# Performance work log

Measured on AMD Instinct MI355X. Metric: run time of the kernel, lower is better.

Reference implementation:

```python
import jax, jax.numpy as jnp
import numpy as np

L, MODS, D, R, B, T = 2, 3, 512, 32, 16, 512  # nlayers, n_modals, embed_dim, rank, batch, length
BETA = 0.1


def setup_inputs() -> dict:
    key = jax.random.key(0)
    ks = jax.random.split(key, 12)
    s_in = 1.0 / np.sqrt(D)      # nn.Linear default init scale for d->R projections
    s_att = 1.0 / np.sqrt(R * R)  # for (R*R)->d projection

    def w(k, shape, scale):
        return jax.random.uniform(k, shape, jnp.float32, -scale, scale)

    return {
        "x_a": jax.random.normal(ks[0], (B, T, D), jnp.float32),
        "x_t": jax.random.normal(ks[1], (B, T, D), jnp.float32),
        "x_v": jax.random.normal(ks[2], (B, T, D), jnp.float32),
        # stacked per-layer, per-modality params
        "Wq1": w(ks[3], (L, MODS, D, R), s_in), "bq1": w(ks[4], (L, MODS, R), s_in),
        "Wq2": w(ks[5], (L, MODS, D, R), s_in), "bq2": w(ks[6], (L, MODS, R), s_in),
        "Wk1": w(ks[7], (L, MODS, D, R), s_in), "bk1": w(ks[8], (L, MODS, R), s_in),
        "Wk2": w(ks[9], (L, MODS, D, R), s_in), "bk2": w(ks[10], (L, MODS, R), s_in),
        "Watt": w(ks[11], (L, MODS, R * R, D), s_att),
        "batt": jnp.zeros((L, MODS, D), jnp.float32),
    }


def _proj(X, W, b):
    # X: [M,B,T,D], W: [M,D,R], b: [M,R] -> [M,B,T,R]
    return jnp.einsum('mbtd,mdr->mbtr', X, W) + b[:, None, None, :]


def reference(x_a, x_t, x_v, Wq1, bq1, Wq2, bq2, Wk1, bk1, Wk2, bk2, Watt, batt):
    X = jnp.stack([x_a, x_t, x_v])  # [M,B,T,D]
    for li in range(L):
        q1 = _proj(X, Wq1[li], bq1[li])
        q2 = _proj(X, Wq2[li], bq2[li])
        k1 = _proj(X, Wk1[li], bk1[li])
        k2 = _proj(X, Wk2[li], bk2[li])
        # low-rank bilinear maps: G_qk[j] = (q1 outer q2) * (k1 outer k2) -> [M,B,T,R,R]
        G = (q1[..., :, None] * q2[..., None, :]) * (k1[..., :, None] * k2[..., None, :])
        Mqk = G.mean(axis=2)  # [M,B,R,R] mean over time
        outs = []
        for j in range(MODS):
            # chained cross-modal contraction == G_j @ (prod_{l!=j, ascending} M_l)
            P = None
            for l in range(MODS):
                if l == j:
                    continue
                P = Mqk[l] if P is None else jnp.einsum('bkl,blo->bko', P, Mqk[l])
            att = jnp.einsum('btkl,blo->btko', G[j], P)  # [B,T,R,R]
            flat = att.reshape(B, T, R * R)
            proj = flat @ Watt[li, j] + batt[li, j]  # [B,T,D]
            outs.append(proj * X[j] + BETA * X[j])  # residual combine (dropout is eval-mode identity)
        X = jnp.stack(outs)
    return X[0], X[1], X[2]
```

## Files before the change

### kernel.cpp

```cpp
#include <hip/hip_runtime.h>

#define L_ 2
#define MODS_ 3
#define D_ 512
#define R_ 32
#define B_ 16
#define T_ 512
#define BT_ (B_*T_)
#define BETA_ 0.1f

typedef _Float16 h8 __attribute__((ext_vector_type(8)));
typedef __fp16   fp16x2 __attribute__((ext_vector_type(2)));
typedef float f32x16 __attribute__((ext_vector_type(16)));

typedef __attribute__((address_space(3))) unsigned int lds_u32;
typedef __attribute__((address_space(1))) const unsigned int glb_u32;

__device__ __forceinline__ void gload_lds16(const uint4* gsrc, uint4* ldst){
    __builtin_amdgcn_global_load_lds((glb_u32*)gsrc, (lds_u32*)ldst, 16, 0, 0);
}

__device__ __forceinline__ h8 mk_h8(float f0,float f1,float f2,float f3,
                                    float f4,float f5,float f6,float f7){
    union { h8 v; fp16x2 p[4]; } r;
    r.p[0] = __builtin_amdgcn_cvt_pkrtz(f0,f1);
    r.p[1] = __builtin_amdgcn_cvt_pkrtz(f2,f3);
    r.p[2] = __builtin_amdgcn_cvt_pkrtz(f4,f5);
    r.p[3] = __builtin_amdgcn_cvt_pkrtz(f6,f7);
    return r.v;
}

__global__ __launch_bounds__(256) void k_cvt(
    const float* __restrict__ Watt,
    const float* __restrict__ Wq1, const float* __restrict__ Wk1,
    const float* __restrict__ Wq2, const float* __restrict__ Wk2,
    uint4* __restrict__ WattF, uint4* __restrict__ WprojF)
{
    const int t = blockIdx.x*256 + threadIdx.x;
    const int NWATT = 6*32*16*2*64;
    if (t < NWATT) {
        const int lane = t & 63, f = t >> 6;
        const int kh = f & 1, nb = (f>>1)&15, s = (f>>5)&31, lj = f>>10;
        const int col  = nb*32 + (lane&31);
        const int row0 = s*32 + kh*16 + (lane>>5)*8;
        const float* src = Watt + ((size_t)lj*1024)*D_ + col;
        union { uint4 q; unsigned short us[8]; } o;
        #pragma unroll
        for (int i=0;i<8;i++){
            float x = src[(size_t)(row0+i)*D_];
            o.us[i] = __builtin_bit_cast(unsigned short, (_Float16)x);
        }
        WattF[t] = o.q;
    } else {
        const int t2 = t - NWATT;
        const int lane = t2 & 63, f = t2 >> 6;
        const int nb = f & 3, s = (f>>2)&31, lm = f>>7;
        const float* Ws = (nb==0)?Wq1:(nb==1)?Wk1:(nb==2)?Wq2:Wk2;
        const int r  = lane&31;
        const int k0 = s*16 + (lane>>5)*8;
        const float* src = Ws + ((size_t)lm*D_)*R_ + r;
        union { uint4 q; unsigned short us[8]; } o;
        #pragma unroll
        for (int i=0;i<8;i++){
            float x = src[(size_t)(k0+i)*R_];
            o.us[i] = __builtin_bit_cast(unsigned short, (_Float16)x);
        }
        WprojF[t2] = o.q;
    }
}

__global__ __launch_bounds__(256) void k_proj_mfma(
    const float* __restrict__ X, const uint4* __restrict__ WprojF,
    const float* __restrict__ bq1, const float* __restrict__ bq2,
    const float* __restrict__ bk1, const float* __restrict__ bk2,
    float* __restrict__ U, float* __restrict__ V, int li)
{
    __shared__ uint4 sm[2][256];
    const int tid = threadIdx.x;
    const int wid = tid>>6, lane = tid&63;
    const int lh = lane>>5, lr = lane&31;
    const int tokg = wid&1, colh = wid>>1;
    const int m = blockIdx.y;
    const int tok0 = blockIdx.x*64;
    const int lm = li*MODS_ + m;
    const int t = tok0 + tokg*32 + lr;

    const uint4* src  = WprojF + (size_t)lm*8192;
    const float* Xrow = X + ((size_t)m*BT_ + t)*D_;

    f32x16 acc0, acc1;
    #pragma unroll
    for (int i=0;i<16;i++){ acc0[i]=0.f; acc1[i]=0.f; }

    gload_lds16(src + tid, &sm[0][wid*64]);
    __syncthreads();

    float4 x0 = *(const float4*)&Xrow[lh*8];
    float4 x1 = *(const float4*)&Xrow[lh*8+4];

    #pragma unroll
    for (int s=0;s<32;s++){
        const int cur = s&1;
        float4 nx0, nx1;
        if (s<31){
            gload_lds16(src + (s+1)*256 + tid, &sm[cur^1][wid*64]);
            nx0 = *(const float4*)&Xrow[(s+1)*16 + lh*8];
            nx1 = *(const float4*)&Xrow[(s+1)*16 + lh*8 + 4];
        }
        h8 a  = mk_h8(x0.x,x0.y,x0.z,x0.w, x1.x,x1.y,x1.z,x1.w);
        h8 b0 = __builtin_bit_cast(h8, sm[cur][(colh*2+0)*64 + lane]);
        h8 b1 = __builtin_bit_cast(h8, sm[cur][(colh*2+1)*64 + lane]);
        acc0 = __builtin_amdgcn_mfma_f32_32x32x16_f16(a, b0, acc0, 0,0,0);
        acc1 = __builtin_amdgcn_mfma_f32_32x32x16_f16(a, b1, acc1, 0,0,0);
        __syncthreads();
        if (s<31){ x0 = nx0; x1 = nx1; }
    }

    const float bA = (colh==0 ? bq1 : bq2)[lm*R_ + lr];
    const float bB = (colh==0 ? bk1 : bk2)[lm*R_ + lr];
    float* Out = (colh==0 ? U : V);
    #pragma unroll
    for (int reg=0;reg<16;reg++){
        const int row = (reg&3) + 8*(reg>>2) + 4*lh;
        const int tt  = tok0 + tokg*32 + row;
        Out[((size_t)m*BT_ + tt)*R_ + lr] = (acc0[reg]+bA)*(acc1[reg]+bB);
    }
}

__global__ __launch_bounds__(256) void k_mqk(const float* __restrict__ U,
                                             const float* __restrict__ V,
                                             float* __restrict__ Mqk)
{
    const int tid = threadIdx.x;
    const int mb  = blockIdx.x;

    __shared__ float Us[64][32];
    __shared__ float Vs[64][32];

    const int l = tid & 31;
    const int g = tid >> 5;
    float acc[4] = {0.f, 0.f, 0.f, 0.f};

    const float* Ub = U + (size_t)mb * T_ * R_;
    const float* Vb = V + (size_t)mb * T_ * R_;
    const int st = tid >> 2, sc = (tid & 3) * 8;

    for (int t0 = 0; t0 < T_; t0 += 64) {
        const float4 u0 = *(const float4*)&Ub[(size_t)(t0 + st) * R_ + sc];
        const float4 u1 = *(const float4*)&Ub[(size_t)(t0 + st) * R_ + sc + 4];
        const float4 v0 = *(const float4*)&Vb[(size_t)(t0 + st) * R_ + sc];
        const float4 v1 = *(const float4*)&Vb[(size_t)(t0 + st) * R_ + sc + 4];
        __syncthreads();
        *(float4*)&Us[st][sc]     = u0; *(float4*)&Us[st][sc + 4] = u1;
        *(float4*)&Vs[st][sc]     = v0; *(float4*)&Vs[st][sc + 4] = v1;
        __syncthreads();
        #pragma unroll
        for (int tt = 0; tt < 64; ++tt) {
            const float v = Vs[tt][l];
            #pragma unroll
            for (int i = 0; i < 4; ++i) acc[i] += Us[tt][g + 8 * i] * v;
        }
    }
    #pragma unroll
    for (int i = 0; i < 4; ++i)
        Mqk[(size_t)mb * (R_ * R_) + (size_t)(g + 8 * i) * R_ + l] = acc[i] * (1.0f / T_);
}

__global__ __launch_bounds__(256) void k_pmat(const float* __restrict__ Mqk,
                                              float* __restrict__ P)
{
    const int tid = threadIdx.x;
    const int j = blockIdx.x, b = blockIdx.y;
    const int a = (j == 0) ? 1 : 0;
    const int c = (j == 2) ? 1 : 2;

    __shared__ float As[32][32];
    __shared__ float Cs[32][32];

    const float4 av = *(const float4*)&Mqk[((size_t)(a * B_ + b)) * 1024 + tid * 4];
    const float4 cv = *(const float4*)&Mqk[((size_t)(c * B_ + b)) * 1024 + tid * 4];
    *(float4*)&(((float*)As)[tid * 4]) = av;
    *(float4*)&(((float*)Cs)[tid * 4]) = cv;
    __syncthreads();

    const int o = tid & 31, g = tid >> 5;
    float acc[4] = {0.f, 0.f, 0.f, 0.f};
    #pragma unroll
    for (int l = 0; l < 32; ++l) {
        const float cvv = Cs[l][o];
        #pragma unroll
        for (int i = 0; i < 4; ++i) acc[i] += As[g + 8 * i][l] * cvv;
    }
    #pragma unroll
    for (int i = 0; i < 4; ++i)
        P[((size_t)(j * B_ + b)) * 1024 + (size_t)(g + 8 * i) * R_ + o] = acc[i];
}

__global__ __launch_bounds__(256) void k_wvec(const float* __restrict__ V,
                                              const float* __restrict__ P,
                                              float* __restrict__ W2)
{
    const int tid  = threadIdx.x;
    const int m    = blockIdx.y;
    const int tok0 = blockIdx.x * 128;
    const int b    = tok0 / T_;

    __shared__ float Ps[32][32];
    __shared__ float Vs[128][32];

    *(float4*)&(((float*)Ps)[tid * 4]) =
        *(const float4*)&P[((size_t)(m * B_ + b)) * 1024 + tid * 4];

    const int st = tid >> 1, sc = (tid & 1) * 16;
    const float* Vb = V + ((size_t)m * BT_ + tok0) * R_;
    #pragma unroll
    for (int q = 0; q < 4; ++q)
        *(float4*)&Vs[st][sc + q * 4] = *(const float4*)&Vb[(size_t)st * R_ + sc + q * 4];
    __syncthreads();

    const int o = tid & 31, g = tid >> 5;
    float* W2b = W2 + ((size_t)m * BT_ + tok0) * R_;
    #pragma unroll
    for (int i = 0; i < 16; ++i) {
        const int t = g * 16 + i;
        float acc = 0.f;
        #pragma unroll
        for (int l = 0; l < 32; ++l) acc += Vs[t][l] * Ps[l][o];
        W2b[(size_t)t * R_ + o] = acc;
    }
}

__global__ __launch_bounds__(256) void k_gemm2_mfma(
    const float* __restrict__ U, const float* __restrict__ W2,
    const uint4* __restrict__ WattF, const float* __restrict__ batt,
    float* __restrict__ X, int li)
{
    __shared__ uint4 sm[2][1024];
    const int tid = threadIdx.x;
    const int wid = tid>>6, lane = tid&63;
    const int lh = lane>>5, lr = lane&31;
    const int tokg = wid&1, colg = wid>>1;
    const int j = blockIdx.z;
    const int tok0 = blockIdx.x*64;
    const int nbB = blockIdx.y*8;
    const int t = tok0 + tokg*32 + lr;

    const uint4* src = WattF + (size_t)(li*MODS_ + j)*65536 + (size_t)nbB*128;

    const float* Urow = U  + ((size_t)j*BT_ + t)*R_;
    const float* Wrow = W2 + ((size_t)j*BT_ + t)*R_;
    float u_r[32];
    #pragma unroll
    for (int q=0;q<8;q++){
        float4 t4 = *(const float4*)&Urow[q*4];
        u_r[q*4+0]=t4.x; u_r[q*4+1]=t4.y; u_r[q*4+2]=t4.z; u_r[q*4+3]=t4.w;
    }
    const float4 wa0 = *(const float4*)&Wrow[lh*8];
    const float4 wa1 = *(const float4*)&Wrow[lh*8+4];
    const float4 wb0 = *(const float4*)&Wrow[16+lh*8];
    const float4 wb1 = *(const float4*)&Wrow[16+lh*8+4];

    f32x16 acc[4];
    #pragma unroll
    for (int n=0;n<4;n++){
        #pragma unroll
        for (int i=0;i<16;i++) acc[n][i]=0.f;
    }

    #pragma unroll
    for (int it=0;it<4;it++)
        gload_lds16(src + it*256 + tid, &sm[0][it*256 + wid*64]);
    __syncthreads();

    #pragma unroll
    for (int s=0;s<32;s++){
        const int cur = s&1;
        if (s<31){
            const uint4* ssrc = src + (size_t)(s+1)*2048;
            #pragma unroll
            for (int it=0;it<4;it++)
                gload_lds16(ssrc + it*256 + tid, &sm[cur^1][it*256 + wid*64]);
        }
        const float us = u_r[s];
        h8 a0 = mk_h8(us*wa0.x,us*wa0.y,us*wa0.z,us*wa0.w,
                      us*wa1.x,us*wa1.y,us*wa1.z,us*wa1.w);
        h8 a1 = mk_h8(us*wb0.x,us*wb0.y,us*wb0.z,us*wb0.w,
                      us*wb1.x,us*wb1.y,us*wb1.z,us*wb1.w);
        #pragma unroll
        for (int n=0;n<4;n++){
            h8 b0 = __builtin_bit_cast(h8, sm[cur][(colg*4+n)*128 +      lane]);
            h8 b1 = __builtin_bit_cast(h8, sm[cur][(colg*4+n)*128 + 64 + lane]);
            acc[n] = __builtin_amdgcn_mfma_f32_32x32x16_f16(a0, b0, acc[n], 0,0,0);
            acc[n] = __builtin_amdgcn_mfma_f32_32x32x16_f16(a1, b1, acc[n], 0,0,0);
        }
        __syncthreads();
    }

    const float* battp = batt + (size_t)(li*MODS_ + j)*D_;
    #pragma unroll
    for (int n=0;n<4;n++){
        const int d  = (nbB + colg*4 + n)*32 + lr;
        const float bt = battp[d];
        #pragma unroll
        for (int reg=0; reg<16; ++reg){
            const int row = (reg&3) + 8*(reg>>2) + 4*lh;
            const size_t xi = ((size_t)j*BT_ + tok0 + tokg*32 + row)*D_ + d;
            const float xv = X[xi];
            X[xi] = (acc[n][reg] + bt)*xv + BETA_*xv;
        }
    }
}

extern "C" void kernel_launch(void* const* d_in, const int* in_sizes, int n_in,
                              void* d_out, int out_size, void* d_ws, size_t ws_size,
                              hipStream_t stream)
{
    const float* x_a  = (const float*)d_in[0];
    const float* x_t  = (const float*)d_in[1];
    const float* x_v  = (const float*)d_in[2];
    const float* Wq1  = (const float*)d_in[3];
    const float* bq1  = (const float*)d_in[4];
    const float* Wq2  = (const float*)d_in[5];
    const float* bq2  = (const float*)d_in[6];
    const float* Wk1  = (const float*)d_in[7];
    const float* bk1  = (const float*)d_in[8];
    const float* Wk2  = (const float*)d_in[9];
    const float* bk2  = (const float*)d_in[10];
    const float* Watt = (const float*)d_in[11];
    const float* batt = (const float*)d_in[12];

    float* X  = (float*)d_out;
    float* U  = (float*)d_ws;
    float* V  = U  + (size_t)MODS_ * BT_ * R_;
    float* W2 = V  + (size_t)MODS_ * BT_ * R_;
    float* Mq = W2 + (size_t)MODS_ * BT_ * R_;
    float* P  = Mq + (size_t)MODS_ * B_ * R_ * R_;
    uint4* WattF  = (uint4*)(P + (size_t)MODS_ * B_ * R_ * R_);
    uint4* WprojF = WattF + 393216;

    const size_t modbytes = (size_t)BT_ * D_ * sizeof(float);
    (void)hipMemcpyAsync(X,                        x_a, modbytes, hipMemcpyDeviceToDevice, stream);
    (void)hipMemcpyAsync(X + (size_t)BT_ * D_,     x_t, modbytes, hipMemcpyDeviceToDevice, stream);
    (void)hipMemcpyAsync(X + (size_t)2 * BT_ * D_, x_v, modbytes, hipMemcpyDeviceToDevice, stream);

    k_cvt<<<1728, 256, 0, stream>>>(Watt, Wq1, Wk1, Wq2, Wk2, WattF, WprojF);

    for (int li = 0; li < L_; ++li) {
        k_proj_mfma<<<dim3(BT_/64, MODS_), 256, 0, stream>>>(
            X, WprojF, bq1, bq2, bk1, bk2, U, V, li);
        k_mqk<<<dim3(MODS_ * B_), 256, 0, stream>>>(U, V, Mq);
        k_pmat<<<dim3(MODS_, B_), 256, 0, stream>>>(Mq, P);
        k_wvec<<<dim3(BT_/128, MODS_), 256, 0, stream>>>(V, P, W2);
        k_gemm2_mfma<<<dim3(BT_/64, D_/256, MODS_), 256, 0, stream>>>(
            U, W2, WattF, batt, X, li);
    }
}
```

Baseline: 318.3 us.

## Store intermediates in fp16, split mqk over time, drop input copies and LDS staging

Stores the U, V and W2 intermediates as scaled fp16 instead of fp32, which cuts their memory traffic. The time-mean reduction is split across eight partial blocks, with the summing folded into k_pmat. Layer 0 reads the input tensors directly, so the three device memcpys go away. Both MFMA kernels now load weights straight into registers with double buffering instead of staging them through LDS behind barriers. The fixed 64x scale factors add an fp16 overflow or precision risk, and register pressure rises in the gemm2 kernel.

```diff
diff --git a/kernel.cpp b/kernel.cpp
--- a/kernel.cpp
+++ b/kernel.cpp
@@ -13,13 +13,6 @@
 typedef __fp16   fp16x2 __attribute__((ext_vector_type(2)));
 typedef float f32x16 __attribute__((ext_vector_type(16)));
 
-typedef __attribute__((address_space(3))) unsigned int lds_u32;
-typedef __attribute__((address_space(1))) const unsigned int glb_u32;
-
-__device__ __forceinline__ void gload_lds16(const uint4* gsrc, uint4* ldst){
-    __builtin_amdgcn_global_load_lds((glb_u32*)gsrc, (lds_u32*)ldst, 16, 0, 0);
-}
-
 __device__ __forceinline__ h8 mk_h8(float f0,float f1,float f2,float f3,
                                     float f4,float f5,float f6,float f7){
     union { h8 v; fp16x2 p[4]; } r;
@@ -28,6 +21,13 @@
     r.p[2] = __builtin_amdgcn_cvt_pkrtz(f4,f5);
     r.p[3] = __builtin_amdgcn_cvt_pkrtz(f6,f7);
     return r.v;
+}
+
+__device__ __forceinline__ float h2f(unsigned short x){
+    return (float)__builtin_bit_cast(_Float16, x);
+}
+__device__ __forceinline__ unsigned short f2h(float x){
+    return __builtin_bit_cast(unsigned short, (_Float16)x);
 }
 
 __global__ __launch_bounds__(256) void k_cvt(
@@ -46,10 +46,7 @@
         const float* src = Watt + ((size_t)lj*1024)*D_ + col;
         union { uint4 q; unsigned short us[8]; } o;
         #pragma unroll
-        for (int i=0;i<8;i++){
-            float x = src[(size_t)(row0+i)*D_];
-            o.us[i] = __builtin_bit_cast(unsigned short, (_Float16)x);
-        }
+        for (int i=0;i<8;i++) o.us[i] = f2h(src[(size_t)(row0+i)*D_]);
         WattF[t] = o.q;
     } else {
         const int t2 = t - NWATT;
@@ -61,21 +58,19 @@
         const float* src = Ws + ((size_t)lm*D_)*R_ + r;
         union { uint4 q; unsigned short us[8]; } o;
         #pragma unroll
-        for (int i=0;i<8;i++){
-            float x = src[(size_t)(k0+i)*R_];
-            o.us[i] = __builtin_bit_cast(unsigned short, (_Float16)x);
-        }
+        for (int i=0;i<8;i++) o.us[i] = f2h(src[(size_t)(k0+i)*R_]);
         WprojF[t2] = o.q;
     }
 }
 
 __global__ __launch_bounds__(256) void k_proj_mfma(
-    const float* __restrict__ X, const uint4* __restrict__ WprojF,
+    const float* __restrict__ xa, const float* __restrict__ xt,
+    const float* __restrict__ xv, const float* __restrict__ X,
+    const uint4* __restrict__ WprojF,
     const float* __restrict__ bq1, const float* __restrict__ bq2,
     const float* __restrict__ bk1, const float* __restrict__ bk2,
-    float* __restrict__ U, float* __restrict__ V, int li)
-{
-    __shared__ uint4 sm[2][256];
+    unsigned short* __restrict__ U16, unsigned short* __restrict__ V16, int li)
+{
     const int tid = threadIdx.x;
     const int wid = tid>>6, lane = tid&63;
     const int lh = lane>>5, lr = lane&31;
@@ -85,120 +80,122 @@
     const int lm = li*MODS_ + m;
     const int t = tok0 + tokg*32 + lr;
 
-    const uint4* src  = WprojF + (size_t)lm*8192;
-    const float* Xrow = X + ((size_t)m*BT_ + t)*D_;
+    const float* Xbase = (li==0) ? (m==0?xa:(m==1?xt:xv)) : (X + (size_t)m*BT_*D_);
+    const float* Xrow  = Xbase + (size_t)t*D_;
+    const uint4* src   = WprojF + (size_t)lm*8192 + (colh*2)*64 + lane;
 
     f32x16 acc0, acc1;
     #pragma unroll
     for (int i=0;i<16;i++){ acc0[i]=0.f; acc1[i]=0.f; }
 
-    gload_lds16(src + tid, &sm[0][wid*64]);
-    __syncthreads();
-
+    uint4 bc0 = src[0], bc1 = src[64];
+    uint4 bn0, bn1;
     float4 x0 = *(const float4*)&Xrow[lh*8];
     float4 x1 = *(const float4*)&Xrow[lh*8+4];
+    float4 nx0, nx1;
 
     #pragma unroll
     for (int s=0;s<32;s++){
-        const int cur = s&1;
-        float4 nx0, nx1;
         if (s<31){
-            gload_lds16(src + (s+1)*256 + tid, &sm[cur^1][wid*64]);
+            bn0 = src[(s+1)*256];
+            bn1 = src[(s+1)*256 + 64];
             nx0 = *(const float4*)&Xrow[(s+1)*16 + lh*8];
             nx1 = *(const float4*)&Xrow[(s+1)*16 + lh*8 + 4];
         }
-        h8 a  = mk_h8(x0.x,x0.y,x0.z,x0.w, x1.x,x1.y,x1.z,x1.w);
-        h8 b0 = __builtin_bit_cast(h8, sm[cur][(colh*2+0)*64 + lane]);
-        h8 b1 = __builtin_bit_cast(h8, sm[cur][(colh*2+1)*64 + lane]);
-        acc0 = __builtin_amdgcn_mfma_f32_32x32x16_f16(a, b0, acc0, 0,0,0);
-        acc1 = __builtin_amdgcn_mfma_f32_32x32x16_f16(a, b1, acc1, 0,0,0);
-        __syncthreads();
-        if (s<31){ x0 = nx0; x1 = nx1; }
+        h8 a = mk_h8(x0.x,x0.y,x0.z,x0.w, x1.x,x1.y,x1.z,x1.w);
+        acc0 = __builtin_amdgcn_mfma_f32_32x32x16_f16(a, __builtin_bit_cast(h8,bc0), acc0, 0,0,0);
+        acc1 = __builtin_amdgcn_mfma_f32_32x32x16_f16(a, __builtin_bit_cast(h8,bc1), acc1, 0,0,0);
+        if (s<31){ bc0=bn0; bc1=bn1; x0=nx0; x1=nx1; }
     }
 
     const float bA = (colh==0 ? bq1 : bq2)[lm*R_ + lr];
     const float bB = (colh==0 ? bk1 : bk2)[lm*R_ + lr];
-    float* Out = (colh==0 ? U : V);
+    unsigned short* Out = (colh==0 ? U16 : V16);
     #pragma unroll
     for (int reg=0;reg<16;reg++){
         const int row = (reg&3) + 8*(reg>>2) + 4*lh;
         const int tt  = tok0 + tokg*32 + row;
-        Out[((size_t)m*BT_ + tt)*R_ + lr] = (acc0[reg]+bA)*(acc1[reg]+bB);
-    }
-}
-
-__global__ __launch_bounds__(256) void k_mqk(const float* __restrict__ U,
-                                             const float* __restrict__ V,
-                                             float* __restrict__ Mqk)
+        const float val = (acc0[reg]+bA)*(acc1[reg]+bB)*64.f;
+        Out[((size_t)m*BT_ + tt)*R_ + lr] = f2h(val);
+    }
+}
+
+__global__ __launch_bounds__(256) void k_mqk_part(
+    const unsigned short* __restrict__ U16,
+    const unsigned short* __restrict__ V16,
+    float* __restrict__ Mqp)
 {
     const int tid = threadIdx.x;
     const int mb  = blockIdx.x;
-
-    __shared__ float Us[64][32];
-    __shared__ float Vs[64][32];
+    const int p   = blockIdx.y;
+    const int t0  = p*64;
+
+    __shared__ unsigned short Us[64][32];
+    __shared__ unsigned short Vs[64][32];
+
+    const int srow = tid>>2, sq = (tid&3)*8;
+    const size_t base = (size_t)mb*T_*R_ + (size_t)(t0+srow)*R_ + sq;
+    *(uint4*)&Us[srow][sq] = *(const uint4*)&U16[base];
+    *(uint4*)&Vs[srow][sq] = *(const uint4*)&V16[base];
+    __syncthreads();
 
     const int l = tid & 31;
     const int g = tid >> 5;
-    float acc[4] = {0.f, 0.f, 0.f, 0.f};
-
-    const float* Ub = U + (size_t)mb * T_ * R_;
-    const float* Vb = V + (size_t)mb * T_ * R_;
-    const int st = tid >> 2, sc = (tid & 3) * 8;
-
-    for (int t0 = 0; t0 < T_; t0 += 64) {
-        const float4 u0 = *(const float4*)&Ub[(size_t)(t0 + st) * R_ + sc];
-        const float4 u1 = *(const float4*)&Ub[(size_t)(t0 + st) * R_ + sc + 4];
-        const float4 v0 = *(const float4*)&Vb[(size_t)(t0 + st) * R_ + sc];
-        const float4 v1 = *(const float4*)&Vb[(size_t)(t0 + st) * R_ + sc + 4];
-        __syncthreads();
-        *(float4*)&Us[st][sc]     = u0; *(float4*)&Us[st][sc + 4] = u1;
-        *(float4*)&Vs[st][sc]     = v0; *(float4*)&Vs[st][sc + 4] = v1;
-        __syncthreads();
-        #pragma unroll
-        for (int tt = 0; tt < 64; ++tt) {
-            const float v = Vs[tt][l];
-            #pragma unroll
-            for (int i = 0; i < 4; ++i) acc[i] += Us[tt][g + 8 * i] * v;
-        }
-    }
-    #pragma unroll
-    for (int i = 0; i < 4; ++i)
-        Mqk[(size_t)mb * (R_ * R_) + (size_t)(g + 8 * i) * R_ + l] = acc[i] * (1.0f / T_);
-}
-
-__global__ __launch_bounds__(256) void k_pmat(const float* __restrict__ Mqk,
+    float acc[4] = {0.f,0.f,0.f,0.f};
+    #pragma unroll 8
+    for (int tt=0; tt<64; ++tt){
+        const float vv = h2f(Vs[tt][l]);
+        #pragma unroll
+        for (int i=0;i<4;i++) acc[i] += h2f(Us[tt][g+8*i]) * vv;
+    }
+    float* out = Mqp + ((size_t)p*48 + mb)*1024;
+    #pragma unroll
+    for (int i=0;i<4;i++) out[(g+8*i)*R_ + l] = acc[i];
+}
+
+__global__ __launch_bounds__(256) void k_pmat(const float* __restrict__ Mqp,
                                               float* __restrict__ P)
 {
     const int tid = threadIdx.x;
     const int j = blockIdx.x, b = blockIdx.y;
     const int a = (j == 0) ? 1 : 0;
     const int c = (j == 2) ? 1 : 2;
+    const float sc = 1.0f/(4096.0f*(float)T_);
 
     __shared__ float As[32][32];
     __shared__ float Cs[32][32];
 
-    const float4 av = *(const float4*)&Mqk[((size_t)(a * B_ + b)) * 1024 + tid * 4];
-    const float4 cv = *(const float4*)&Mqk[((size_t)(c * B_ + b)) * 1024 + tid * 4];
-    *(float4*)&(((float*)As)[tid * 4]) = av;
-    *(float4*)&(((float*)Cs)[tid * 4]) = cv;
+    float4 sa = {0,0,0,0}, scv = {0,0,0,0};
+    #pragma unroll
+    for (int p=0;p<8;p++){
+        const float4 pa = *(const float4*)&Mqp[((size_t)p*48 + a*B_+b)*1024 + tid*4];
+        const float4 pc = *(const float4*)&Mqp[((size_t)p*48 + c*B_+b)*1024 + tid*4];
+        sa.x+=pa.x; sa.y+=pa.y; sa.z+=pa.z; sa.w+=pa.w;
+        scv.x+=pc.x; scv.y+=pc.y; scv.z+=pc.z; scv.w+=pc.w;
+    }
+    sa.x*=sc; sa.y*=sc; sa.z*=sc; sa.w*=sc;
+    scv.x*=sc; scv.y*=sc; scv.z*=sc; scv.w*=sc;
+    *(float4*)&(((float*)As)[tid*4]) = sa;
+    *(float4*)&(((float*)Cs)[tid*4]) = scv;
     __syncthreads();
 
     const int o = tid & 31, g = tid >> 5;
-    float acc[4] = {0.f, 0.f, 0.f, 0.f};
+    float acc[4] = {0.f,0.f,0.f,0.f};
     #pragma unroll
     for (int l = 0; l < 32; ++l) {
         const float cvv = Cs[l][o];
         #pragma unroll
-        for (int i = 0; i < 4; ++i) acc[i] += As[g + 8 * i][l] * cvv;
+        for (int i = 0; i < 4; ++i) acc[i] += As[g + 8*i][l] * cvv;
     }
     #pragma unroll
     for (int i = 0; i < 4; ++i)
-        P[((size_t)(j * B_ + b)) * 1024 + (size_t)(g + 8 * i) * R_ + o] = acc[i];
-}
-
-__global__ __launch_bounds__(256) void k_wvec(const float* __restrict__ V,
-                                              const float* __restrict__ P,
-                                              float* __restrict__ W2)
+        P[((size_t)(j*B_ + b))*1024 + (size_t)(g + 8*i)*R_ + o] = acc[i];
+}
+
+__global__ __launch_bounds__(256) void k_wvec(
+    const unsigned short* __restrict__ V16,
+    const float* __restrict__ P,
+    unsigned short* __restrict__ W16)
 {
     const int tid  = threadIdx.x;
     const int m    = blockIdx.y;
@@ -206,36 +203,39 @@
     const int b    = tok0 / T_;
 
     __shared__ float Ps[32][32];
-    __shared__ float Vs[128][32];
-
-    *(float4*)&(((float*)Ps)[tid * 4]) =
-        *(const float4*)&P[((size_t)(m * B_ + b)) * 1024 + tid * 4];
-
-    const int st = tid >> 1, sc = (tid & 1) * 16;
-    const float* Vb = V + ((size_t)m * BT_ + tok0) * R_;
-    #pragma unroll
-    for (int q = 0; q < 4; ++q)
-        *(float4*)&Vs[st][sc + q * 4] = *(const float4*)&Vb[(size_t)st * R_ + sc + q * 4];
+    __shared__ unsigned short Vs[128][32];
+
+    *(float4*)&(((float*)Ps)[tid*4]) =
+        *(const float4*)&P[((size_t)(m*B_ + b))*1024 + tid*4];
+
+    const unsigned short* Vb = V16 + ((size_t)m*BT_ + tok0)*R_;
+    #pragma unroll
+    for (int e=0;e<2;e++){
+        const int k = tid*2 + e;
+        *(uint4*)&Vs[k>>2][(k&3)*8] = *(const uint4*)&Vb[(size_t)(k>>2)*R_ + (k&3)*8];
+    }
     __syncthreads();
 
     const int o = tid & 31, g = tid >> 5;
-    float* W2b = W2 + ((size_t)m * BT_ + tok0) * R_;
+    unsigned short* Wb = W16 + ((size_t)m*BT_ + tok0)*R_;
     #pragma unroll
     for (int i = 0; i < 16; ++i) {
-        const int t = g * 16 + i;
+        const int t = g*16 + i;
         float acc = 0.f;
         #pragma unroll
-        for (int l = 0; l < 32; ++l) acc += Vs[t][l] * Ps[l][o];
-        W2b[(size_t)t * R_ + o] = acc;
+        for (int l = 0; l < 32; ++l) acc += h2f(Vs[t][l]) * Ps[l][o];
+        Wb[(size_t)t*R_ + o] = f2h(acc);
     }
 }
 
 __global__ __launch_bounds__(256) void k_gemm2_mfma(
-    const float* __restrict__ U, const float* __restrict__ W2,
+    const unsigned short* __restrict__ U16,
+    const unsigned short* __restrict__ W16,
     const uint4* __restrict__ WattF, const float* __restrict__ batt,
+    const float* __restrict__ xa, const float* __restrict__ xt,
+    const float* __restrict__ xv,
     float* __restrict__ X, int li)
 {
-    __shared__ uint4 sm[2][1024];
     const int tid = threadIdx.x;
     const int wid = tid>>6, lane = tid&63;
     const int lh = lane>>5, lr = lane&31;
@@ -245,20 +245,20 @@
     const int nbB = blockIdx.y*8;
     const int t = tok0 + tokg*32 + lr;
 
-    const uint4* src = WattF + (size_t)(li*MODS_ + j)*65536 + (size_t)nbB*128;
-
-    const float* Urow = U  + ((size_t)j*BT_ + t)*R_;
-    const float* Wrow = W2 + ((size_t)j*BT_ + t)*R_;
-    float u_r[32];
-    #pragma unroll
-    for (int q=0;q<8;q++){
-        float4 t4 = *(const float4*)&Urow[q*4];
-        u_r[q*4+0]=t4.x; u_r[q*4+1]=t4.y; u_r[q*4+2]=t4.z; u_r[q*4+3]=t4.w;
-    }
-    const float4 wa0 = *(const float4*)&Wrow[lh*8];
-    const float4 wa1 = *(const float4*)&Wrow[lh*8+4];
-    const float4 wb0 = *(const float4*)&Wrow[16+lh*8];
-    const float4 wb1 = *(const float4*)&Wrow[16+lh*8+4];
+    const uint4* src = WattF + (size_t)(li*MODS_ + j)*65536
+                             + (size_t)(nbB + colg*4)*128 + lane;
+
+    union { uint4 q[4]; __fp16 h[32]; } uu;
+    {
+        const uint4* Ur = (const uint4*)(U16 + ((size_t)j*BT_ + t)*R_);
+        uu.q[0]=Ur[0]; uu.q[1]=Ur[1]; uu.q[2]=Ur[2]; uu.q[3]=Ur[3];
+    }
+    union { uint4 q; fp16x2 p[4]; } wa, wb;
+    {
+        const uint4* Wr = (const uint4*)(W16 + ((size_t)j*BT_ + t)*R_);
+        wa.q = Wr[lh];
+        wb.q = Wr[2+lh];
+    }
 
     f32x16 acc[4];
     #pragma unroll
@@ -267,36 +267,47 @@
         for (int i=0;i<16;i++) acc[n][i]=0.f;
     }
 
-    #pragma unroll
-    for (int it=0;it<4;it++)
-        gload_lds16(src + it*256 + tid, &sm[0][it*256 + wid*64]);
-    __syncthreads();
-
-    #pragma unroll
-    for (int s=0;s<32;s++){
-        const int cur = s&1;
-        if (s<31){
-            const uint4* ssrc = src + (size_t)(s+1)*2048;
-            #pragma unroll
-            for (int it=0;it<4;it++)
-                gload_lds16(ssrc + it*256 + tid, &sm[cur^1][it*256 + wid*64]);
-        }
-        const float us = u_r[s];
-        h8 a0 = mk_h8(us*wa0.x,us*wa0.y,us*wa0.z,us*wa0.w,
-                      us*wa1.x,us*wa1.y,us*wa1.z,us*wa1.w);
-        h8 a1 = mk_h8(us*wb0.x,us*wb0.y,us*wb0.z,us*wb0.w,
-                      us*wb1.x,us*wb1.y,us*wb1.z,us*wb1.w);
-        #pragma unroll
-        for (int n=0;n<4;n++){
-            h8 b0 = __builtin_bit_cast(h8, sm[cur][(colg*4+n)*128 +      lane]);
-            h8 b1 = __builtin_bit_cast(h8, sm[cur][(colg*4+n)*128 + 64 + lane]);
-            acc[n] = __builtin_amdgcn_mfma_f32_32x32x16_f16(a0, b0, acc[n], 0,0,0);
-            acc[n] = __builtin_amdgcn_mfma_f32_32x32x16_f16(a1, b1, acc[n], 0,0,0);
-        }
-        __syncthreads();
+    uint4 bufA[8], bufB[8];
+    #pragma unroll
+    for (int f=0;f<8;f++) bufA[f] = src[(f>>1)*128 + (f&1)*64];
+
+    #pragma unroll
+    for (int s2=0; s2<16; ++s2){
+        const int s = 2*s2;
+        #pragma unroll
+        for (int f=0;f<8;f++) bufB[f] = src[(size_t)(s+1)*2048 + (f>>1)*128 + (f&1)*64];
+        {
+            fp16x2 us2; us2[0] = uu.h[s]; us2[1] = uu.h[s];
+            union { h8 v; fp16x2 p[4]; } a0, a1;
+            #pragma unroll
+            for (int q=0;q<4;q++){ a0.p[q] = us2*wa.p[q]; a1.p[q] = us2*wb.p[q]; }
+            #pragma unroll
+            for (int n=0;n<4;n++){
+                acc[n] = __builtin_amdgcn_mfma_f32_32x32x16_f16(a0.v, __builtin_bit_cast(h8,bufA[2*n  ]), acc[n], 0,0,0);
+                acc[n] = __builtin_amdgcn_mfma_f32_32x32x16_f16(a1.v, __builtin_bit_cast(h8,bufA[2*n+1]), acc[n], 0,0,0);
+            }
+        }
+        if (s+2 < 32){
+            #pragma unroll
+            for (int f=0;f<8;f++) bufA[f] = src[(size_t)(s+2)*2048 + (f>>1)*128 + (f&1)*64];
+        }
+        {
+            fp16x2 us2; us2[0] = uu.h[s+1]; us2[1] = uu.h[s+1];
+            union { h8 v; fp16x2 p[4]; } a0, a1;
+            #pragma unroll
+            for (int q=0;q<4;q++){ a0.p[q] = us2*wa.p[q]; a1.p[q] = us2*wb.p[q]; }
+            #pragma unroll
+            for (int n=0;n<4;n++){
+                acc[n] = __builtin_amdgcn_mfma_f32_32x32x16_f16(a0.v, __builtin_bit_cast(h8,bufB[2*n  ]), acc[n], 0,0,0);
+                acc[n] = __builtin_amdgcn_mfma_f32_32x32x16_f16(a1.v, __builtin_bit_cast(h8,bufB[2*n+1]), acc[n], 0,0,0);
+            }
+        }
     }
 
     const float* battp = batt + (size_t)(li*MODS_ + j)*D_;
+    const float* Xin = (li==0) ? (j==0?xa:(j==1?xt:xv)) : (X + (size_t)j*BT_*D_);
+    float* Xout = X + (size_t)j*BT_*D_;
+    const float inv = 1.0f/4096.0f;
     #pragma unroll
     for (int n=0;n<4;n++){
         const int d  = (nbB + colg*4 + n)*32 + lr;
@@ -304,9 +315,9 @@
         #pragma unroll
         for (int reg=0; reg<16; ++reg){
             const int row = (reg&3) + 8*(reg>>2) + 4*lh;
-            const size_t xi = ((size_t)j*BT_ + tok0 + tokg*32 + row)*D_ + d;
-            const float xv = X[xi];
-            X[xi] = (acc[n][reg] + bt)*xv + BETA_*xv;
+            const size_t xi = (size_t)(tok0 + tokg*32 + row)*D_ + d;
+            const float xvv = Xin[xi];
+            Xout[xi] = (acc[n][reg]*inv + bt)*xvv + BETA_*xvv;
         }
     }
 }
@@ -329,29 +340,25 @@
     const float* Watt = (const float*)d_in[11];
     const float* batt = (const float*)d_in[12];
 
-    float* X  = (float*)d_out;
-    float* U  = (float*)d_ws;
-    float* V  = U  + (size_t)MODS_ * BT_ * R_;
-    float* W2 = V  + (size_t)MODS_ * BT_ * R_;
-    float* Mq = W2 + (size_t)MODS_ * BT_ * R_;
-    float* P  = Mq + (size_t)MODS_ * B_ * R_ * R_;
-    uint4* WattF  = (uint4*)(P + (size_t)MODS_ * B_ * R_ * R_);
+    float* X = (float*)d_out;
+
+    uint4* WattF  = (uint4*)d_ws;
     uint4* WprojF = WattF + 393216;
-
-    const size_t modbytes = (size_t)BT_ * D_ * sizeof(float);
-    (void)hipMemcpyAsync(X,                        x_a, modbytes, hipMemcpyDeviceToDevice, stream);
-    (void)hipMemcpyAsync(X + (size_t)BT_ * D_,     x_t, modbytes, hipMemcpyDeviceToDevice, stream);
-    (void)hipMemcpyAsync(X + (size_t)2 * BT_ * D_, x_v, modbytes, hipMemcpyDeviceToDevice, stream);
+    float* Mqp    = (float*)(WprojF + 49152);
+    float* P      = Mqp + 393216;
+    unsigned short* U16 = (unsigned short*)(P + 49152);
+    unsigned short* V16 = U16 + (size_t)MODS_*BT_*R_;
+    unsigned short* W16 = V16 + (size_t)MODS_*BT_*R_;
 
     k_cvt<<<1728, 256, 0, stream>>>(Watt, Wq1, Wk1, Wq2, Wk2, WattF, WprojF);
 
     for (int li = 0; li < L_; ++li) {
         k_proj_mfma<<<dim3(BT_/64, MODS_), 256, 0, stream>>>(
-            X, WprojF, bq1, bq2, bk1, bk2, U, V, li);
-        k_mqk<<<dim3(MODS_ * B_), 256, 0, stream>>>(U, V, Mq);
-        k_pmat<<<dim3(MODS_, B_), 256, 0, stream>>>(Mq, P);
-        k_wvec<<<dim3(BT_/128, MODS_), 256, 0, stream>>>(V, P, W2);
+            x_a, x_t, x_v, X, WprojF, bq1, bq2, bk1, bk2, U16, V16, li);
+        k_mqk_part<<<dim3(MODS_*B_, 8), 256, 0, stream>>>(U16, V16, Mqp);
+        k_pmat<<<dim3(MODS_, B_), 256, 0, stream>>>(Mqp, P);
+        k_wvec<<<dim3(BT_/128, MODS_), 256, 0, stream>>>(V16, P, W16);
         k_gemm2_mfma<<<dim3(BT_/64, D_/256, MODS_), 256, 0, stream>>>(
-            U, W2, WattF, batt, X, li);
-    }
-}
+            U16, W16, WattF, batt, x_a, x_t, x_v, X, li);
+    }
+}
```

After: 396.2 us. 24.5% more time.
